# Kernel optimization log

Hardware: AMD Instinct MI355X
Metric: run time of the kernel (lower is better)

The kernel has to match this reference:

```python
import jax, jax.numpy as jnp
import numpy as np

B, T, C, H = 4, 4096, 768, 64  # batch, seq, embed_size, head_size


def setup_inputs() -> dict:
    key = jax.random.key(0)
    kx, kq, kk, kv = jax.random.split(key, 4)
    s = 1.0 / np.sqrt(C)
    return {
        "x": jax.random.normal(kx, (B, T, C), dtype=jnp.float32),
        "Wq": jax.random.normal(kq, (C, H), dtype=jnp.float32) * s,
        "Wk": jax.random.normal(kk, (C, H), dtype=jnp.float32) * s,
        "Wv": jax.random.normal(kv, (C, H), dtype=jnp.float32) * s,
    }


def reference(x, Wq, Wk, Wv):
    Bx, Tx, Cx = x.shape
    Q = x @ Wq  # [B, T, H]
    K = x @ Wk
    V = x @ Wv
    # NOTE: original scales by sqrt(C) = sqrt(embed_size), not head_size
    scores = jnp.einsum('bqh,bkh->bqk', Q, K) / jnp.sqrt(jnp.asarray(Cx, x.dtype))
    causal = jnp.tril(jnp.ones((Tx, Tx), dtype=bool))
    scores = jnp.where(causal, scores, -jnp.inf)
    weights = jax.nn.softmax(scores, axis=-1)
    # dropout = identity in eval mode
    return jnp.einsum('bqk,bkh->bqh', weights, V)
```

## Files before the change

kernel.cpp:

```cpp
#include <hip/hip_runtime.h>

typedef __bf16 bf16x8 __attribute__((ext_vector_type(8)));
typedef float f32x4 __attribute__((ext_vector_type(4)));

#define MFMA16(a,b,c) __builtin_amdgcn_mfma_f32_16x16x32_bf16(a,b,c,0,0,0)

__device__ __forceinline__ unsigned short f2b(float x){
  __bf16 b = (__bf16)x;
  return __builtin_bit_cast(unsigned short, b);
}
__device__ __forceinline__ float b2f(unsigned short u){
  return __builtin_bit_cast(float, ((unsigned)u)<<16);
}

__device__ __forceinline__ void gld16(const void* g, void* l){
  __builtin_amdgcn_global_load_lds(
      (const __attribute__((address_space(1))) unsigned int*)g,
      (__attribute__((address_space(3))) unsigned int*)l, 16, 0, 0);
}

__global__ __launch_bounds__(256) void pack_w(const float* __restrict__ Wq,
                                              const float* __restrict__ Wk,
                                              const float* __restrict__ Wv,
                                              unsigned short* __restrict__ Wt){
  int idx = blockIdx.x*256 + threadIdx.x;
  int n = idx/768, c = idx - n*768;
  const float* W = (n < 64) ? Wq : ((n < 128) ? Wk : Wv);
  Wt[n*768 + c] = f2b(W[c*64 + (n & 63)]);
}

__global__ __launch_bounds__(256,2) void qkv_proj(const float* __restrict__ x,
                                                  const unsigned short* __restrict__ Wt,
                                                  unsigned short* __restrict__ Qb,
                                                  unsigned short* __restrict__ Kb,
                                                  unsigned short* __restrict__ Vt){
  __shared__ __attribute__((aligned(16))) float Xl[2][32*64];
  __shared__ __attribute__((aligned(16))) unsigned short Wl[2][192*64];
  const int tid = threadIdx.x;
  const int w = tid>>6, l = tid&63, quad = l>>4, lr = l&15;
  const int row0 = blockIdx.x*32;

  auto stage = [&](int kk, int buf){
#pragma unroll
    for(int i=0;i<2;i++){
      int n = (w*2+i)*4 + (l>>4);
      int sc = (l&15) ^ (n&15);
      gld16(x + (size_t)(row0+n)*768 + kk*64 + sc*4, &Xl[buf][(w*2+i)*256]);
    }
#pragma unroll
    for(int i=0;i<6;i++){
      int gr0 = (w*6+i)*8;
      int n = gr0 + (l>>3);
      int sc = (l&7) ^ (l>>3);
      gld16(Wt + (size_t)n*768 + kk*64 + sc*8, &Wl[buf][gr0*64]);
    }
  };

  f32x4 acc[2][3];
#pragma unroll
  for(int mt=0;mt<2;mt++)
#pragma unroll
    for(int nt=0;nt<3;nt++) acc[mt][nt] = (f32x4)0.0f;

  stage(0, 0);
  int buf = 0;
  for(int kk=0; kk<12; kk++){
    __syncthreads();
    if(kk+1 < 12) stage(kk+1, buf^1);
    bf16x8 a[2][2];
#pragma unroll
    for(int mt=0;mt<2;mt++){
#pragma unroll
      for(int ks=0;ks<2;ks++){
        int c = ks*8 + quad*2;
        f32x4 v0 = *(const f32x4*)&Xl[buf][(mt*16+lr)*64 + ((c   ^ lr)&15)*4];
        f32x4 v1 = *(const f32x4*)&Xl[buf][(mt*16+lr)*64 + (((c+1)^ lr)&15)*4];
#pragma unroll
        for(int jj=0;jj<4;jj++){ a[mt][ks][jj] = (__bf16)v0[jj]; a[mt][ks][4+jj] = (__bf16)v1[jj]; }
      }
    }
#pragma unroll
    for(int nt=0;nt<3;nt++){
#pragma unroll
      for(int ks=0;ks<2;ks++){
        int n = w*48 + nt*16 + lr;
        int q = ks*4 + quad;
        bf16x8 bfr = *(const bf16x8*)&Wl[buf][n*64 + ((q ^ (lr&7))&7)*8];
#pragma unroll
        for(int mt=0;mt<2;mt++) acc[mt][nt] = MFMA16(a[mt][ks], bfr, acc[mt][nt]);
      }
    }
    buf ^= 1;
  }
  const int b_ = row0>>12;
  const float sc = 0.03608439182435161f;
#pragma unroll
  for(int mt=0;mt<2;mt++){
    const int t0 = (row0 & 4095) + mt*16 + quad*4;
#pragma unroll
    for(int nt=0;nt<3;nt++){
      int g = w*48 + nt*16 + lr;
      if(g < 64){
#pragma unroll
        for(int r=0;r<4;r++) Qb[((size_t)(b_*4096 + t0 + r))*64 + g] = f2b(acc[mt][nt][r]*sc);
      } else if(g < 128){
#pragma unroll
        for(int r=0;r<4;r++) Kb[((size_t)(b_*4096 + t0 + r))*64 + (g-64)] = f2b(acc[mt][nt][r]);
      } else {
        ushort4 pk;
        pk.x = f2b(acc[mt][nt][0]); pk.y = f2b(acc[mt][nt][1]);
        pk.z = f2b(acc[mt][nt][2]); pk.w = f2b(acc[mt][nt][3]);
        *(ushort4*)&Vt[((size_t)(b_*64 + (g-128)))*4096 + t0] = pk;
      }
    }
  }
}

__device__ __forceinline__ void attn_stage(const unsigned short* kbp, const unsigned short* vbp,
                                           int kt, int w, int r8, int cj,
                                           unsigned short* Kl, unsigned short* Vl){
#pragma unroll
  for(int i=0;i<2;i++){
    int row = w*16 + i*8 + r8;
    int gc = cj ^ r8;
    gld16(kbp + ((size_t)(kt*64 + row))*64 + gc*8, Kl + (w*16 + i*8)*64);
    gld16(vbp + ((size_t)row)*4096 + kt*64 + gc*8, Vl + (w*16 + i*8)*64);
  }
}

__global__ __launch_bounds__(256,2) void attn(const unsigned short* __restrict__ Qb,
                                              const unsigned short* __restrict__ Kb,
                                              const unsigned short* __restrict__ Vt,
                                              unsigned short* __restrict__ Opart,
                                              float* __restrict__ Rpart){
  __shared__ __attribute__((aligned(16))) unsigned short Kl[2][64*64];
  __shared__ __attribute__((aligned(16))) unsigned short Vl[2][64*64];
  __shared__ __attribute__((aligned(16))) unsigned short Pl[4][32*72];
  const int tid = threadIdx.x;
  const int w = tid>>6, l = tid&63, quad = l>>4, lr = l&15;
  const int xx = 143 - blockIdx.x;
  int i = 0, accu = 0;
  while(true){ int c = (i+4)>>2; if(accu + c > xx) break; accu += c; i++; }
  const int r = xx - accu;
  const int b = blockIdx.y;
  const int q0 = i*128;
  const int lo = r*8;
  const int hi = min(lo+8, 2*i+2);
  const int diag0 = 2*i;
  const int r8 = l>>3, cj = l&7;
  const int lx = lr & 7;
  bf16x8 aq[2][2];
#pragma unroll
  for(int m=0;m<2;m++){
    const unsigned short* qp = Qb + ((size_t)(b*4096 + q0 + w*32 + m*16 + lr))*64 + quad*8;
    aq[m][0] = *(const bf16x8*)qp;
    aq[m][1] = *(const bf16x8*)(qp + 32);
  }
  f32x4 o_[2][4];
#pragma unroll
  for(int m=0;m<2;m++)
#pragma unroll
    for(int nt=0;nt<4;nt++) o_[m][nt] = (f32x4)0.0f;
  float rs[2][4] = {{0.f,0.f,0.f,0.f},{0.f,0.f,0.f,0.f}};
  const unsigned short* kbp = Kb + ((size_t)b*4096)*64;
  const unsigned short* vbp = Vt + ((size_t)b*64)*4096;
  unsigned short* pw = &Pl[w][0];

  attn_stage(kbp, vbp, lo, w, r8, cj, Kl[0], Vl[0]);
  int cur = 0;
  for(int kt = lo; kt < hi; kt++){
    __syncthreads();
    if(kt+1 < hi) attn_stage(kbp, vbp, kt+1, w, r8, cj, Kl[cur^1], Vl[cur^1]);
    f32x4 s4[2][4];
#pragma unroll
    for(int ct=0;ct<4;ct++){
      int base = (ct*16+lr)*64;
      bf16x8 b0 = *(const bf16x8*)&Kl[cur][base + ((quad    ^ lx)<<3)];
      bf16x8 b1 = *(const bf16x8*)&Kl[cur][base + (((4+quad)^ lx)<<3)];
#pragma unroll
      for(int m=0;m<2;m++){
        f32x4 z = (f32x4)0.0f;
        z = MFMA16(aq[m][0], b0, z);
        s4[m][ct] = MFMA16(aq[m][1], b1, z);
      }
    }
    if(kt >= diag0){
#pragma unroll
      for(int m=0;m<2;m++){
        int qg = q0 + w*32 + m*16 + quad*4;
#pragma unroll
        for(int ct=0;ct<4;ct++){
          int kg = kt*64 + ct*16 + lr;
#pragma unroll
          for(int rr=0;rr<4;rr++){
            float p = (kg <= qg + rr) ? __expf(s4[m][ct][rr]) : 0.0f;
            rs[m][rr] += p;
            pw[(m*16+quad*4+rr)*72 + ct*16 + lr] = f2b(p);
          }
        }
      }
    } else {
#pragma unroll
      for(int m=0;m<2;m++){
#pragma unroll
        for(int ct=0;ct<4;ct++){
#pragma unroll
          for(int rr=0;rr<4;rr++){
            float p = __expf(s4[m][ct][rr]);
            rs[m][rr] += p;
            pw[(m*16+quad*4+rr)*72 + ct*16 + lr] = f2b(p);
          }
        }
      }
    }
#pragma unroll
    for(int ks=0;ks<2;ks++){
      bf16x8 ap[2];
#pragma unroll
      for(int m=0;m<2;m++) ap[m] = *(const bf16x8*)&pw[(m*16+lr)*72 + ks*32 + quad*8];
#pragma unroll
      for(int nt=0;nt<4;nt++){
        bf16x8 bv = *(const bf16x8*)&Vl[cur][(nt*16+lr)*64 + (((ks*4+quad)^lx)<<3)];
#pragma unroll
        for(int m=0;m<2;m++) o_[m][nt] = MFMA16(ap[m], bv, o_[m][nt]);
      }
    }
    cur ^= 1;
  }
  const int slab = r*4 + b;
#pragma unroll
  for(int m=0;m<2;m++){
#pragma unroll
    for(int rr=0;rr<4;rr++){
      float t = rs[m][rr];
#pragma unroll
      for(int off=1; off<16; off<<=1) t += __shfl_xor(t, off, 16);
      int row = q0 + w*32 + m*16 + quad*4 + rr;
      if(lr == 0) Rpart[slab*4096 + row] = t;
#pragma unroll
      for(int nt=0;nt<4;nt++)
        Opart[((size_t)(slab*4096 + row))*64 + nt*16 + lr] = f2b(o_[m][nt][rr]);
    }
  }
}

__global__ __launch_bounds__(256) void combine(const unsigned short* __restrict__ Opart,
                                               const float* __restrict__ Rpart,
                                               float* __restrict__ out){
  int gid = blockIdx.x*256 + threadIdx.x;
  int cg = gid & 15;
  int t  = (gid >> 4) & 4095;
  int b  = gid >> 16;
  int i  = t >> 7;
  int np = (i + 4) >> 2;
  float o0=0.f, o1=0.f, o2=0.f, o3=0.f, rsum=0.f;
  for(int r=0; r<np; r++){
    int slab = r*4 + b;
    rsum += Rpart[slab*4096 + t];
    ushort4 u = *(const ushort4*)(Opart + ((size_t)(slab*4096 + t))*64 + cg*4);
    o0 += b2f(u.x); o1 += b2f(u.y); o2 += b2f(u.z); o3 += b2f(u.w);
  }
  float inv = 1.0f/rsum;
  f32x4 v; v[0]=o0*inv; v[1]=o1*inv; v[2]=o2*inv; v[3]=o3*inv;
  *(f32x4*)(out + ((size_t)(b*4096 + t))*64 + cg*4) = v;
}

extern "C" void kernel_launch(void* const* d_in, const int* in_sizes, int n_in,
                              void* d_out, int out_size, void* d_ws, size_t ws_size,
                              hipStream_t stream){
  const float* x  = (const float*)d_in[0];
  const float* Wq = (const float*)d_in[1];
  const float* Wk = (const float*)d_in[2];
  const float* Wv = (const float*)d_in[3];
  float* out = (float*)d_out;
  char* ws = (char*)d_ws;
  unsigned short* Wt = (unsigned short*)(ws);
  unsigned short* Qb = (unsigned short*)(ws + 0x080000);
  unsigned short* Kb = (unsigned short*)(ws + 0x280000);
  unsigned short* Vt = (unsigned short*)(ws + 0x480000);
  unsigned short* Opart = (unsigned short*)(ws + 0x680000);
  float* Rpart = (float*)(ws + 0x1680000);
  hipLaunchKernelGGL(pack_w,   dim3(576),     dim3(256), 0, stream, Wq, Wk, Wv, Wt);
  hipLaunchKernelGGL(qkv_proj, dim3(512),     dim3(256), 0, stream, x, Wt, Qb, Kb, Vt);
  hipLaunchKernelGGL(attn,     dim3(144, 4),  dim3(256), 0, stream, Qb, Kb, Vt, Opart, Rpart);
  hipLaunchKernelGGL(combine,  dim3(1024),    dim3(256), 0, stream, Opart, Rpart, out);
}
```

Baseline: 128.3 us.

## Keep P in registers via transposed MFMA and halve key-split chunk size

The score MFMA operands are swapped so S comes out transposed, letting each lane pack its exp'd probabilities directly into the B operand of a 16x16x16 bf16 MFMA for the PV product. This removes the per-wave LDS staging buffer for P along with its stores and reloads. Separately, each block now handles 4 key tiles instead of 8, so the grid grows from 144 to 272 blocks per batch for better load balance. The cost is more partial slabs to write and to combine, plus a larger workspace region.

Result: slower. 131.0 us (+2.1%).

```diff
diff --git a/kernel.cpp b/kernel.cpp
--- a/kernel.cpp
+++ b/kernel.cpp
@@ -2,8 +2,10 @@
 
 typedef __bf16 bf16x8 __attribute__((ext_vector_type(8)));
 typedef float f32x4 __attribute__((ext_vector_type(4)));
-
-#define MFMA16(a,b,c) __builtin_amdgcn_mfma_f32_16x16x32_bf16(a,b,c,0,0,0)
+typedef short s16x4 __attribute__((ext_vector_type(4)));
+
+#define MFMA16(a,b,c)    __builtin_amdgcn_mfma_f32_16x16x32_bf16(a,b,c,0,0,0)
+#define MFMA16K16(a,b,c) __builtin_amdgcn_mfma_f32_16x16x16bf16_1k(a,b,c,0,0,0)
 
 __device__ __forceinline__ unsigned short f2b(float x){
   __bf16 b = (__bf16)x;
@@ -135,17 +137,16 @@
                                               float* __restrict__ Rpart){
   __shared__ __attribute__((aligned(16))) unsigned short Kl[2][64*64];
   __shared__ __attribute__((aligned(16))) unsigned short Vl[2][64*64];
-  __shared__ __attribute__((aligned(16))) unsigned short Pl[4][32*72];
   const int tid = threadIdx.x;
   const int w = tid>>6, l = tid&63, quad = l>>4, lr = l&15;
-  const int xx = 143 - blockIdx.x;
+  const int xx = 271 - blockIdx.x;
   int i = 0, accu = 0;
-  while(true){ int c = (i+4)>>2; if(accu + c > xx) break; accu += c; i++; }
+  while(true){ int c = (i+2)>>1; if(accu + c > xx) break; accu += c; i++; }
   const int r = xx - accu;
   const int b = blockIdx.y;
   const int q0 = i*128;
-  const int lo = r*8;
-  const int hi = min(lo+8, 2*i+2);
+  const int lo = r*4;
+  const int hi = min(lo+4, 2*i+2);
   const int diag0 = 2*i;
   const int r8 = l>>3, cj = l&7;
   const int lx = lr & 7;
@@ -161,10 +162,9 @@
   for(int m=0;m<2;m++)
 #pragma unroll
     for(int nt=0;nt<4;nt++) o_[m][nt] = (f32x4)0.0f;
-  float rs[2][4] = {{0.f,0.f,0.f,0.f},{0.f,0.f,0.f,0.f}};
+  float rs[2] = {0.f, 0.f};
   const unsigned short* kbp = Kb + ((size_t)b*4096)*64;
   const unsigned short* vbp = Vt + ((size_t)b*64)*4096;
-  unsigned short* pw = &Pl[w][0];
 
   attn_stage(kbp, vbp, lo, w, r8, cj, Kl[0], Vl[0]);
   int cur = 0;
@@ -180,23 +180,28 @@
 #pragma unroll
       for(int m=0;m<2;m++){
         f32x4 z = (f32x4)0.0f;
-        z = MFMA16(aq[m][0], b0, z);
-        s4[m][ct] = MFMA16(aq[m][1], b1, z);
-      }
-    }
+        z = MFMA16(b0, aq[m][0], z);
+        s4[m][ct] = MFMA16(b1, aq[m][1], z);
+      }
+    }
+    s16x4 bp[2][4];
     if(kt >= diag0){
 #pragma unroll
       for(int m=0;m<2;m++){
-        int qg = q0 + w*32 + m*16 + quad*4;
+        int qg = q0 + w*32 + m*16 + lr;
 #pragma unroll
         for(int ct=0;ct<4;ct++){
-          int kg = kt*64 + ct*16 + lr;
+          float p[4];
 #pragma unroll
           for(int rr=0;rr<4;rr++){
-            float p = (kg <= qg + rr) ? __expf(s4[m][ct][rr]) : 0.0f;
-            rs[m][rr] += p;
-            pw[(m*16+quad*4+rr)*72 + ct*16 + lr] = f2b(p);
+            int kg = kt*64 + ct*16 + quad*4 + rr;
+            p[rr] = (kg <= qg) ? __expf(s4[m][ct][rr]) : 0.0f;
+            rs[m] += p[rr];
           }
+          int2 pk;
+          pk.x = (int)((unsigned)f2b(p[0]) | ((unsigned)f2b(p[1])<<16));
+          pk.y = (int)((unsigned)f2b(p[2]) | ((unsigned)f2b(p[3])<<16));
+          bp[m][ct] = __builtin_bit_cast(s16x4, pk);
         }
       }
     } else {
@@ -204,25 +209,27 @@
       for(int m=0;m<2;m++){
 #pragma unroll
         for(int ct=0;ct<4;ct++){
+          float p[4];
 #pragma unroll
           for(int rr=0;rr<4;rr++){
-            float p = __expf(s4[m][ct][rr]);
-            rs[m][rr] += p;
-            pw[(m*16+quad*4+rr)*72 + ct*16 + lr] = f2b(p);
+            p[rr] = __expf(s4[m][ct][rr]);
+            rs[m] += p[rr];
           }
+          int2 pk;
+          pk.x = (int)((unsigned)f2b(p[0]) | ((unsigned)f2b(p[1])<<16));
+          pk.y = (int)((unsigned)f2b(p[2]) | ((unsigned)f2b(p[3])<<16));
+          bp[m][ct] = __builtin_bit_cast(s16x4, pk);
         }
       }
     }
 #pragma unroll
-    for(int ks=0;ks<2;ks++){
-      bf16x8 ap[2];
-#pragma unroll
-      for(int m=0;m<2;m++) ap[m] = *(const bf16x8*)&pw[(m*16+lr)*72 + ks*32 + quad*8];
+    for(int ct=0;ct<4;ct++){
 #pragma unroll
       for(int nt=0;nt<4;nt++){
-        bf16x8 bv = *(const bf16x8*)&Vl[cur][(nt*16+lr)*64 + (((ks*4+quad)^lx)<<3)];
-#pragma unroll
-        for(int m=0;m<2;m++) o_[m][nt] = MFMA16(ap[m], bv, o_[m][nt]);
+        s16x4 av = *(const s16x4*)&Vl[cur][(nt*16+lr)*64
+                      + (((ct*2 + (quad>>1)) ^ lx)<<3) + (quad&1)*4];
+#pragma unroll
+        for(int m=0;m<2;m++) o_[m][nt] = MFMA16K16(av, bp[m][ct], o_[m][nt]);
       }
     }
     cur ^= 1;
@@ -230,16 +237,17 @@
   const int slab = r*4 + b;
 #pragma unroll
   for(int m=0;m<2;m++){
-#pragma unroll
-    for(int rr=0;rr<4;rr++){
-      float t = rs[m][rr];
-#pragma unroll
-      for(int off=1; off<16; off<<=1) t += __shfl_xor(t, off, 16);
-      int row = q0 + w*32 + m*16 + quad*4 + rr;
-      if(lr == 0) Rpart[slab*4096 + row] = t;
-#pragma unroll
-      for(int nt=0;nt<4;nt++)
-        Opart[((size_t)(slab*4096 + row))*64 + nt*16 + lr] = f2b(o_[m][nt][rr]);
+    float t = rs[m];
+    t += __shfl_xor(t, 16, 64);
+    t += __shfl_xor(t, 32, 64);
+    int row = q0 + w*32 + m*16 + lr;
+    if(quad == 0) Rpart[slab*4096 + row] = t;
+#pragma unroll
+    for(int nt=0;nt<4;nt++){
+      ushort4 pk;
+      pk.x = f2b(o_[m][nt][0]); pk.y = f2b(o_[m][nt][1]);
+      pk.z = f2b(o_[m][nt][2]); pk.w = f2b(o_[m][nt][3]);
+      *(ushort4*)&Opart[((size_t)(slab*4096 + row))*64 + nt*16 + quad*4] = pk;
     }
   }
 }
@@ -252,7 +260,7 @@
   int t  = (gid >> 4) & 4095;
   int b  = gid >> 16;
   int i  = t >> 7;
-  int np = (i + 4) >> 2;
+  int np = (i + 2) >> 1;
   float o0=0.f, o1=0.f, o2=0.f, o3=0.f, rsum=0.f;
   for(int r=0; r<np; r++){
     int slab = r*4 + b;
@@ -279,9 +287,9 @@
   unsigned short* Kb = (unsigned short*)(ws + 0x280000);
   unsigned short* Vt = (unsigned short*)(ws + 0x480000);
   unsigned short* Opart = (unsigned short*)(ws + 0x680000);
-  float* Rpart = (float*)(ws + 0x1680000);
+  float* Rpart = (float*)(ws + 0x2680000);
   hipLaunchKernelGGL(pack_w,   dim3(576),     dim3(256), 0, stream, Wq, Wk, Wv, Wt);
   hipLaunchKernelGGL(qkv_proj, dim3(512),     dim3(256), 0, stream, x, Wt, Qb, Kb, Vt);
-  hipLaunchKernelGGL(attn,     dim3(144, 4),  dim3(256), 0, stream, Qb, Kb, Vt, Opart, Rpart);
+  hipLaunchKernelGGL(attn,     dim3(272, 4),  dim3(256), 0, stream, Qb, Kb, Vt, Opart, Rpart);
   hipLaunchKernelGGL(combine,  dim3(1024),    dim3(256), 0, stream, Opart, Rpart, out);
 }
```
